# Kernel tuning notes

Measured on AMD Instinct MI355X. Metric: run time of the kernel, lower is better.

## Reference

```python
import jax, jax.numpy as jnp
import numpy as np

EPS = 1e-12  # keras K.l2_normalize epsilon


def _l2_normalize(v, axis):
    return v * jax.lax.rsqrt(jnp.maximum(jnp.sum(v * v, axis=axis, keepdims=True), EPS))


def setup_inputs() -> dict:
    key = jax.random.key(0)
    k1, k2, k3, k4 = jax.random.split(key, 4)
    B, T, D, K, O = 32, 1024, 512, 64, 1024
    x = jax.random.normal(k1, (B, T, D), dtype=jnp.float32)
    weight = jax.random.normal(k2, (D, K), dtype=jnp.float32) * (1.0 / np.sqrt(D))
    bias = jnp.zeros((K,), dtype=jnp.float32)
    centers = jax.random.normal(k3, (K, D), dtype=jnp.float32)
    reduc_dim = jax.random.normal(k4, (D * K, O), dtype=jnp.float32) * 0.01
    return {"x": x, "weight": weight, "bias": bias, "centers": centers, "reduc_dim": reduc_dim}


def reference(x, weight, bias, centers, reduc_dim):
    # x: [B,T,D], weight: [D,K], bias: [K]
    # soft assignment: softmax over centers
    a = jax.nn.softmax(jnp.einsum('btd,dk->btk', x, weight) + bias, axis=-1)  # [B,T,K]
    # aggregate descriptors per center: batch_dot over time axis -> [B,K,D]
    x_agg = jnp.einsum('btk,btd->bkd', a, x)
    # total soft weight per center: [B,K]
    sum_w = jnp.sum(a, axis=1)
    # residual vs centers, broadcast: [B,K,D]
    full = x_agg - sum_w[:, :, None] * centers[None, :, :]
    # intra-normalize per center vector
    full = _l2_normalize(full, axis=-1)
    B = x.shape[0]
    full = full.reshape(B, -1)  # [B, K*D]
    full = _l2_normalize(full, axis=-1)
    return full @ reduc_dim  # [B, output_dim]
```

## Files before the change

kernel.cpp:

```cpp
#include <hip/hip_runtime.h>
#include <math.h>

#define TT 1024
#define DD 512
#define KK 64
#define OO 1024
#define EPSF 1e-12f

typedef __attribute__((ext_vector_type(8))) short bf16x8;
typedef __attribute__((ext_vector_type(4))) float f32x4;

__device__ __forceinline__ ushort f2bf(float f) {
  unsigned u = __float_as_uint(f);
  u = (u + 0x7FFFu + ((u >> 16) & 1u)) >> 16;
  return (ushort)u;
}
__device__ __forceinline__ float bf2f(ushort h) {
  return __uint_as_float(((unsigned)h) << 16);
}


__global__ __launch_bounds__(256) void nv_k0(const float* __restrict__ w,
                                             ushort* __restrict__ whT,
                                             float* __restrict__ sum_w) {
  int idx = blockIdx.x * 256 + threadIdx.x;
  if (idx < 32768) {
    int d = idx >> 6, k = idx & 63;
    whT[(size_t)k * DD + d] = f2bf(w[idx]);
  } else if (idx < 32768 + 2048) {
    sum_w[idx - 32768] = 0.f;
  }
}

__global__ __launch_bounds__(256) void nv_k1(
    const float* __restrict__ x, const ushort* __restrict__ whT,
    const float* __restrict__ bias, ushort* __restrict__ aT,
    ushort* __restrict__ xbfT, float* __restrict__ sum_w) {
  const int b = blockIdx.y, t0 = blockIdx.x * 64;
  const int tid = threadIdx.x;
  const int wave = tid >> 6, lane = tid & 63, l15 = lane & 15, q = lane >> 4;

  __shared__ ushort xs[64 * 64];
  __shared__ ushort xsT[64 * 64];
  __shared__ ushort wsm[64 * 64];

  f32x4 acc[4];
#pragma unroll
  for (int nt = 0; nt < 4; ++nt)
#pragma unroll
    for (int r = 0; r < 4; ++r) acc[nt][r] = 0.f;

  for (int dc = 0; dc < DD; dc += 64) {
    __syncthreads();
#pragma unroll
    for (int it = 0; it < 2; ++it) {
      int gi = it * 256 + tid;
      int t = gi >> 3, gd = gi & 7;
      const float* px = x + (size_t)(b * TT + t0 + t) * DD + dc + gd * 8;
      float4 v0 = *(const float4*)px;
      float4 v1 = *(const float4*)(px + 4);
      ushort u[8];
      u[0] = f2bf(v0.x); u[1] = f2bf(v0.y); u[2] = f2bf(v0.z); u[3] = f2bf(v0.w);
      u[4] = f2bf(v1.x); u[5] = f2bf(v1.y); u[6] = f2bf(v1.z); u[7] = f2bf(v1.w);
      bf16x8 pk;
#pragma unroll
      for (int i = 0; i < 8; ++i) pk[i] = (short)u[i];
      *(bf16x8*)(xs + t * 64 + ((gd ^ (t & 7)) << 3)) = pk;
      int tg = t >> 3;
#pragma unroll
      for (int i = 0; i < 8; ++i) {
        int d = gd * 8 + i;
        xsT[d * 64 + ((tg ^ ((d >> 3) & 7)) << 3) + (t & 7)] = u[i];
      }
    }
#pragma unroll
    for (int it = 0; it < 2; ++it) {
      int gi = it * 256 + tid;
      int k = gi >> 3, gd = gi & 7;
      bf16x8 v = *(const bf16x8*)(whT + (size_t)k * DD + dc + gd * 8);
      *(bf16x8*)(wsm + k * 64 + ((gd ^ (k & 7)) << 3)) = v;
    }
    __syncthreads();
#pragma unroll
    for (int kc = 0; kc < 2; ++kc) {
      int gq = kc * 4 + q;
      int t = wave * 16 + l15;
      bf16x8 af = *(const bf16x8*)(xs + t * 64 + ((gq ^ (t & 7)) << 3));
#pragma unroll
      for (int nt = 0; nt < 4; ++nt) {
        int k = nt * 16 + l15;
        bf16x8 bfv = *(const bf16x8*)(wsm + k * 64 + ((gq ^ (k & 7)) << 3));
        acc[nt] = __builtin_amdgcn_mfma_f32_16x16x32_bf16(af, bfv, acc[nt], 0, 0, 0);
      }
    }
#pragma unroll
    for (int it = 0; it < 2; ++it) {
      int gi = it * 256 + tid;
      int d = gi >> 3, g = gi & 7;
      bf16x8 v = *(const bf16x8*)(xsT + d * 64 + (g << 3));
      int tg = g ^ ((d >> 3) & 7);
      *(bf16x8*)(xbfT + (size_t)(b * DD + dc + d) * TT + t0 + tg * 8) = v;
    }
  }

  float bia[4];
#pragma unroll
  for (int nt = 0; nt < 4; ++nt) bia[nt] = bias[nt * 16 + l15];

  ushort au[4][4];
  float sw[4] = {0.f, 0.f, 0.f, 0.f};
#pragma unroll
  for (int r = 0; r < 4; ++r) {
    float l[4];
#pragma unroll
    for (int nt = 0; nt < 4; ++nt) l[nt] = acc[nt][r] + bia[nt];
    float m = fmaxf(fmaxf(l[0], l[1]), fmaxf(l[2], l[3]));
#pragma unroll
    for (int s = 1; s <= 8; s <<= 1) m = fmaxf(m, __shfl_xor(m, s));
    float e[4];
#pragma unroll
    for (int nt = 0; nt < 4; ++nt) e[nt] = __expf(l[nt] - m);
    float ssum = e[0] + e[1] + e[2] + e[3];
#pragma unroll
    for (int s = 1; s <= 8; s <<= 1) ssum += __shfl_xor(ssum, s);
    float inv = 1.f / ssum;
#pragma unroll
    for (int nt = 0; nt < 4; ++nt) {
      ushort u = f2bf(e[nt] * inv);
      au[nt][r] = u;
      sw[nt] += bf2f(u);
    }
  }
#pragma unroll
  for (int nt = 0; nt < 4; ++nt) {
    float s = sw[nt];
    s += __shfl_xor(s, 16);
    s += __shfl_xor(s, 32);
    if (q == 0) atomicAdd(sum_w + b * KK + nt * 16 + l15, s);
  }
  __syncthreads();
#pragma unroll
  for (int nt = 0; nt < 4; ++nt)
#pragma unroll
    for (int r = 0; r < 4; ++r) {
      int k = nt * 16 + l15;
      int t = wave * 16 + q * 4 + r;
      xs[k * 64 + (((t >> 3) ^ (k & 7)) << 3) + (t & 7)] = au[nt][r];
    }
  __syncthreads();
#pragma unroll
  for (int it = 0; it < 2; ++it) {
    int gi = it * 256 + tid;
    int k = gi >> 3, g = gi & 7;
    bf16x8 v = *(const bf16x8*)(xs + k * 64 + (g << 3));
    int tg = g ^ (k & 7);
    *(bf16x8*)(aT + (size_t)(b * KK + k) * TT + t0 + tg * 8) = v;
  }
}

__global__ __launch_bounds__(256) void nv_k2(
    const ushort* __restrict__ aT, const ushort* __restrict__ xbfT,
    float* __restrict__ xaggP) {
  const int d0 = blockIdx.x * 64;
  const int b = blockIdx.y;
  const int tsp = blockIdx.z;
  const int tid = threadIdx.x;
  const int wave = tid >> 6, lane = tid & 63, l15 = lane & 15, q = lane >> 4;

  __shared__ ushort asx[64 * 64];
  __shared__ ushort xsb[64 * 64];

  f32x4 acc[4];
#pragma unroll
  for (int nt = 0; nt < 4; ++nt)
#pragma unroll
    for (int r = 0; r < 4; ++r) acc[nt][r] = 0.f;

  for (int tc = 0; tc < 4; ++tc) {
    const int t0 = tsp * 256 + tc * 64;
    __syncthreads();
#pragma unroll
    for (int it = 0; it < 2; ++it) {
      int gi = it * 256 + tid;
      int k = gi >> 3, g = gi & 7;
      bf16x8 v = *(const bf16x8*)(aT + (size_t)(b * KK + k) * TT + t0 + g * 8);
      *(bf16x8*)(asx + k * 64 + ((g ^ (k & 7)) << 3)) = v;
    }
#pragma unroll
    for (int it = 0; it < 2; ++it) {
      int gi = it * 256 + tid;
      int d = gi >> 3, g = gi & 7;
      bf16x8 v = *(const bf16x8*)(xbfT + (size_t)(b * DD + d0 + d) * TT + t0 + g * 8);
      *(bf16x8*)(xsb + d * 64 + ((g ^ (d & 7)) << 3)) = v;
    }
    __syncthreads();
#pragma unroll
    for (int kc = 0; kc < 2; ++kc) {
      int gq = kc * 4 + q;
      int k = wave * 16 + l15;
      bf16x8 af = *(const bf16x8*)(asx + k * 64 + ((gq ^ (k & 7)) << 3));
#pragma unroll
      for (int nt = 0; nt < 4; ++nt) {
        int d = nt * 16 + l15;
        bf16x8 bfv = *(const bf16x8*)(xsb + d * 64 + ((gq ^ (d & 7)) << 3));
        acc[nt] = __builtin_amdgcn_mfma_f32_16x16x32_bf16(af, bfv, acc[nt], 0, 0, 0);
      }
    }
  }
#pragma unroll
  for (int nt = 0; nt < 4; ++nt)
#pragma unroll
    for (int r = 0; r < 4; ++r) {
      int k = wave * 16 + q * 4 + r;
      xaggP[(size_t)((tsp * 32 + b) * KK + k) * DD + d0 + nt * 16 + l15] = acc[nt][r];
    }
}

__global__ __launch_bounds__(128) void nv_k3a(
    const float* __restrict__ xaggP, float* __restrict__ full,
    const float* __restrict__ centers, const float* __restrict__ sum_w,
    float* __restrict__ s1) {
  const int k = blockIdx.x, b = blockIdx.y;
  const int tid = threadIdx.x;
  const float sw = sum_w[b * KK + k];
  float4 v = make_float4(0.f, 0.f, 0.f, 0.f);
#pragma unroll
  for (int sp = 0; sp < 4; ++sp) {
    float4 p = *((const float4*)(xaggP + (size_t)((sp * 32 + b) * KK + k) * DD) + tid);
    v.x += p.x; v.y += p.y; v.z += p.z; v.w += p.w;
  }
  float4 c = *((const float4*)(centers + (size_t)k * DD) + tid);
  v.x = fmaf(-sw, c.x, v.x);
  v.y = fmaf(-sw, c.y, v.y);
  v.z = fmaf(-sw, c.z, v.z);
  v.w = fmaf(-sw, c.w, v.w);
  *((float4*)(full + (size_t)(b * KK + k) * DD) + tid) = v;
  float ss = v.x * v.x + v.y * v.y + v.z * v.z + v.w * v.w;
#pragma unroll
  for (int s = 1; s <= 32; s <<= 1) ss += __shfl_xor(ss, s);
  __shared__ float red[2];
  if ((tid & 63) == 0) red[tid >> 6] = ss;
  __syncthreads();
  if (tid == 0) s1[b * KK + k] = red[0] + red[1];
}

__global__ __launch_bounds__(64) void nv_k3b(const float* __restrict__ s1,
                                             float* __restrict__ scale) {
  const int b = blockIdx.x, k = threadIdx.x;
  float r = s1[b * KK + k];
  float d1 = fmaxf(r, EPSF);
  float s2 = r / d1;
#pragma unroll
  for (int s = 1; s <= 32; s <<= 1) s2 += __shfl_xor(s2, s);
  scale[b * KK + k] = rsqrtf(d1) * rsqrtf(fmaxf(s2, EPSF));
}

__global__ __launch_bounds__(128) void nv_k3c(const float* __restrict__ full,
                                              const float* __restrict__ scale,
                                              float* __restrict__ fullT) {
  const int blk = blockIdx.x;
  const int b = blk >> 6, k = blk & 63;
  const float sc = scale[blk];
  float4 v = *((const float4*)(full + (size_t)blk * DD) + threadIdx.x);
  int r0 = k * DD + threadIdx.x * 4;
  fullT[(size_t)(r0 + 0) * 32 + b] = v.x * sc;
  fullT[(size_t)(r0 + 1) * 32 + b] = v.y * sc;
  fullT[(size_t)(r0 + 2) * 32 + b] = v.z * sc;
  fullT[(size_t)(r0 + 3) * 32 + b] = v.w * sc;
}

__global__ __launch_bounds__(256, 2) void nv_k4(
    const float* __restrict__ fullT, const float* __restrict__ reduc,
    float* __restrict__ outP) {
  const int strip = blockIdx.x;
  const int ksp = blockIdx.y;
  const int tid = threadIdx.x;
  const int wave = tid >> 6, lane = tid & 63;
  const int c0 = strip * 256 + lane * 4;
  const int kblk = ksp * 256;

  __shared__ float fst[256 * 32];

#pragma unroll
  for (int it = 0; it < 8; ++it) {
    int f4 = it * 256 + tid;
    *(float4*)(fst + f4 * 4) = *(const float4*)(fullT + (size_t)kblk * 32 + f4 * 4);
  }
  __syncthreads();

  float4 acc[32];
#pragma unroll
  for (int b = 0; b < 32; ++b) acc[b] = make_float4(0.f, 0.f, 0.f, 0.f);

  const int kw = wave * 64;
#pragma unroll 2
  for (int kk = 0; kk < 64; ++kk) {
    const int kl = kw + kk;
    float4 rv = *(const float4*)(reduc + (size_t)(kblk + kl) * OO + c0);
#pragma unroll
    for (int b4 = 0; b4 < 8; ++b4) {
      float4 fv = *(const float4*)(fst + kl * 32 + b4 * 4);
      acc[b4 * 4 + 0].x = fmaf(fv.x, rv.x, acc[b4 * 4 + 0].x);
      acc[b4 * 4 + 0].y = fmaf(fv.x, rv.y, acc[b4 * 4 + 0].y);
      acc[b4 * 4 + 0].z = fmaf(fv.x, rv.z, acc[b4 * 4 + 0].z);
      acc[b4 * 4 + 0].w = fmaf(fv.x, rv.w, acc[b4 * 4 + 0].w);
      acc[b4 * 4 + 1].x = fmaf(fv.y, rv.x, acc[b4 * 4 + 1].x);
      acc[b4 * 4 + 1].y = fmaf(fv.y, rv.y, acc[b4 * 4 + 1].y);
      acc[b4 * 4 + 1].z = fmaf(fv.y, rv.z, acc[b4 * 4 + 1].z);
      acc[b4 * 4 + 1].w = fmaf(fv.y, rv.w, acc[b4 * 4 + 1].w);
      acc[b4 * 4 + 2].x = fmaf(fv.z, rv.x, acc[b4 * 4 + 2].x);
      acc[b4 * 4 + 2].y = fmaf(fv.z, rv.y, acc[b4 * 4 + 2].y);
      acc[b4 * 4 + 2].z = fmaf(fv.z, rv.z, acc[b4 * 4 + 2].z);
      acc[b4 * 4 + 2].w = fmaf(fv.z, rv.w, acc[b4 * 4 + 2].w);
      acc[b4 * 4 + 3].x = fmaf(fv.w, rv.x, acc[b4 * 4 + 3].x);
      acc[b4 * 4 + 3].y = fmaf(fv.w, rv.y, acc[b4 * 4 + 3].y);
      acc[b4 * 4 + 3].z = fmaf(fv.w, rv.z, acc[b4 * 4 + 3].z);
      acc[b4 * 4 + 3].w = fmaf(fv.w, rv.w, acc[b4 * 4 + 3].w);
    }
  }

  __syncthreads();
  for (int w = 0; w < 4; ++w) {
    if (wave == w) {
      if (w == 0) {
#pragma unroll
        for (int b = 0; b < 32; ++b)
          *(float4*)(fst + b * 256 + lane * 4) = acc[b];
      } else {
#pragma unroll
        for (int b = 0; b < 32; ++b) {
          float4 v = *(float4*)(fst + b * 256 + lane * 4);
          v.x += acc[b].x; v.y += acc[b].y; v.z += acc[b].z; v.w += acc[b].w;
          *(float4*)(fst + b * 256 + lane * 4) = v;
        }
      }
    }
    __syncthreads();
  }

#pragma unroll
  for (int it = 0; it < 8; ++it) {
    int f4 = it * 256 + tid;
    int b = f4 >> 6, cg = f4 & 63;
    *(float4*)(outP + ((size_t)(ksp * 32 + b) * OO) + strip * 256 + cg * 4) =
        *(const float4*)(fst + b * 256 + cg * 4);
  }
}

__global__ __launch_bounds__(256) void nv_k5(const float* __restrict__ outP,
                                             float* __restrict__ out) {
  const int idx = blockIdx.x * 256 + threadIdx.x;
  float s = 0.f;
#pragma unroll 8
  for (int sp = 0; sp < 128; ++sp) s += outP[(size_t)sp * 32768 + idx];
  out[idx] = s;
}

extern "C" void kernel_launch(void* const* d_in, const int* in_sizes, int n_in,
                              void* d_out, int out_size, void* d_ws, size_t ws_size,
                              hipStream_t stream) {
  const float* x = (const float*)d_in[0];
  const float* weight = (const float*)d_in[1];
  const float* bias = (const float*)d_in[2];
  const float* centers = (const float*)d_in[3];
  const float* reduc = (const float*)d_in[4];
  float* out = (float*)d_out;
  float* ws = (float*)d_ws;

  ushort* aT = (ushort*)ws;
  ushort* xbfT = (ushort*)(ws + 1048576);
  float* xaggP = ws + 9437184;
  float* full = ws + 13631488;
  float* fullT = ws + 14680064;
  float* outP = ws + 15728640;
  ushort* whT = (ushort*)(ws + 19922944);
  float* sum_w = ws + 19922944 + 16384;
  float* s1 = sum_w + 2048;
  float* scale = sum_w + 4096;

  nv_k0<<<136, 256, 0, stream>>>(weight, whT, sum_w);
  nv_k1<<<dim3(16, 32), 256, 0, stream>>>(x, whT, bias, aT, xbfT, sum_w);
  nv_k2<<<dim3(8, 32, 4), 256, 0, stream>>>(aT, xbfT, xaggP);
  nv_k3a<<<dim3(64, 32), 128, 0, stream>>>(xaggP, full, centers, sum_w, s1);
  nv_k3b<<<32, 64, 0, stream>>>(s1, scale);
  nv_k3c<<<2048, 128, 0, stream>>>(full, scale, fullT);
  nv_k4<<<dim3(4, 128), 256, 0, stream>>>(fullT, reduc, outP);
  nv_k5<<<128, 256, 0, stream>>>(outP, out);
}
```

Before: 293.3 us.

## Fuse soft-assignment and aggregation kernels, retile transpose, batch reduc loads

Merges the softmax-assignment kernel and the aggregation GEMM into one kernel. Each block keeps its assignment tile in shared memory and rereads x from global to build a transposed bf16 tile, so the aT and xbfT intermediates are no longer written and read through global memory. The time split doubles to 8 partials, and nv_k3a is widened to sum them. It also rewrites the transpose kernel to use a padded shared-memory tile for coalesced stores, loads four reduc rows per iteration in nv_k4 and drops its occupancy hint, and changes nv_k5 block size. The cost is fewer blocks for the fused kernel (256), reading x twice, and more xaggP partial traffic.

Result: no change. 290.3 us (-1.0%).

```diff
diff --git a/kernel.cpp b/kernel.cpp
--- a/kernel.cpp
+++ b/kernel.cpp
@@ -32,46 +32,43 @@
   }
 }
 
-__global__ __launch_bounds__(256) void nv_k1(
+__global__ __launch_bounds__(256) void nv_k12(
     const float* __restrict__ x, const ushort* __restrict__ whT,
-    const float* __restrict__ bias, ushort* __restrict__ aT,
-    ushort* __restrict__ xbfT, float* __restrict__ sum_w) {
-  const int b = blockIdx.y, t0 = blockIdx.x * 64;
+    const float* __restrict__ bias, float* __restrict__ xaggP,
+    float* __restrict__ sum_w) {
+  const int tsp = blockIdx.x, b = blockIdx.y;
+  const int t0 = tsp * 128;
   const int tid = threadIdx.x;
   const int wave = tid >> 6, lane = tid & 63, l15 = lane & 15, q = lane >> 4;
 
-  __shared__ ushort xs[64 * 64];
-  __shared__ ushort xsT[64 * 64];
+  __shared__ ushort xs[128 * 64];
   __shared__ ushort wsm[64 * 64];
-
-  f32x4 acc[4];
-#pragma unroll
-  for (int nt = 0; nt < 4; ++nt)
-#pragma unroll
-    for (int r = 0; r < 4; ++r) acc[nt][r] = 0.f;
+  __shared__ ushort aTl[64 * 128];
+  __shared__ ushort xsT[64 * 128];
+
+  f32x4 acc[2][4];
+#pragma unroll
+  for (int mt = 0; mt < 2; ++mt)
+#pragma unroll
+    for (int nt = 0; nt < 4; ++nt)
+#pragma unroll
+      for (int r = 0; r < 4; ++r) acc[mt][nt][r] = 0.f;
 
   for (int dc = 0; dc < DD; dc += 64) {
     __syncthreads();
 #pragma unroll
-    for (int it = 0; it < 2; ++it) {
+    for (int it = 0; it < 4; ++it) {
       int gi = it * 256 + tid;
       int t = gi >> 3, gd = gi & 7;
       const float* px = x + (size_t)(b * TT + t0 + t) * DD + dc + gd * 8;
       float4 v0 = *(const float4*)px;
       float4 v1 = *(const float4*)(px + 4);
-      ushort u[8];
-      u[0] = f2bf(v0.x); u[1] = f2bf(v0.y); u[2] = f2bf(v0.z); u[3] = f2bf(v0.w);
-      u[4] = f2bf(v1.x); u[5] = f2bf(v1.y); u[6] = f2bf(v1.z); u[7] = f2bf(v1.w);
       bf16x8 pk;
-#pragma unroll
-      for (int i = 0; i < 8; ++i) pk[i] = (short)u[i];
+      pk[0] = (short)f2bf(v0.x); pk[1] = (short)f2bf(v0.y);
+      pk[2] = (short)f2bf(v0.z); pk[3] = (short)f2bf(v0.w);
+      pk[4] = (short)f2bf(v1.x); pk[5] = (short)f2bf(v1.y);
+      pk[6] = (short)f2bf(v1.z); pk[7] = (short)f2bf(v1.w);
       *(bf16x8*)(xs + t * 64 + ((gd ^ (t & 7)) << 3)) = pk;
-      int tg = t >> 3;
-#pragma unroll
-      for (int i = 0; i < 8; ++i) {
-        int d = gd * 8 + i;
-        xsT[d * 64 + ((tg ^ ((d >> 3) & 7)) << 3) + (t & 7)] = u[i];
-      }
     }
 #pragma unroll
     for (int it = 0; it < 2; ++it) {
@@ -84,22 +81,20 @@
 #pragma unroll
     for (int kc = 0; kc < 2; ++kc) {
       int gq = kc * 4 + q;
-      int t = wave * 16 + l15;
-      bf16x8 af = *(const bf16x8*)(xs + t * 64 + ((gq ^ (t & 7)) << 3));
+      bf16x8 bfv[4];
 #pragma unroll
       for (int nt = 0; nt < 4; ++nt) {
         int k = nt * 16 + l15;
-        bf16x8 bfv = *(const bf16x8*)(wsm + k * 64 + ((gq ^ (k & 7)) << 3));
-        acc[nt] = __builtin_amdgcn_mfma_f32_16x16x32_bf16(af, bfv, acc[nt], 0, 0, 0);
-      }
-    }
-#pragma unroll
-    for (int it = 0; it < 2; ++it) {
-      int gi = it * 256 + tid;
-      int d = gi >> 3, g = gi & 7;
-      bf16x8 v = *(const bf16x8*)(xsT + d * 64 + (g << 3));
-      int tg = g ^ ((d >> 3) & 7);
-      *(bf16x8*)(xbfT + (size_t)(b * DD + dc + d) * TT + t0 + tg * 8) = v;
+        bfv[nt] = *(const bf16x8*)(wsm + k * 64 + ((gq ^ (k & 7)) << 3));
+      }
+#pragma unroll
+      for (int mt = 0; mt < 2; ++mt) {
+        int t = wave * 32 + mt * 16 + l15;
+        bf16x8 af = *(const bf16x8*)(xs + t * 64 + ((gq ^ (t & 7)) << 3));
+#pragma unroll
+        for (int nt = 0; nt < 4; ++nt)
+          acc[mt][nt] = __builtin_amdgcn_mfma_f32_16x16x32_bf16(af, bfv[nt], acc[mt][nt], 0, 0, 0);
+      }
     }
   }
 
@@ -107,30 +102,32 @@
 #pragma unroll
   for (int nt = 0; nt < 4; ++nt) bia[nt] = bias[nt * 16 + l15];
 
-  ushort au[4][4];
+  ushort au[2][4][4];
   float sw[4] = {0.f, 0.f, 0.f, 0.f};
 #pragma unroll
-  for (int r = 0; r < 4; ++r) {
-    float l[4];
-#pragma unroll
-    for (int nt = 0; nt < 4; ++nt) l[nt] = acc[nt][r] + bia[nt];
-    float m = fmaxf(fmaxf(l[0], l[1]), fmaxf(l[2], l[3]));
-#pragma unroll
-    for (int s = 1; s <= 8; s <<= 1) m = fmaxf(m, __shfl_xor(m, s));
-    float e[4];
-#pragma unroll
-    for (int nt = 0; nt < 4; ++nt) e[nt] = __expf(l[nt] - m);
-    float ssum = e[0] + e[1] + e[2] + e[3];
-#pragma unroll
-    for (int s = 1; s <= 8; s <<= 1) ssum += __shfl_xor(ssum, s);
-    float inv = 1.f / ssum;
-#pragma unroll
-    for (int nt = 0; nt < 4; ++nt) {
-      ushort u = f2bf(e[nt] * inv);
-      au[nt][r] = u;
-      sw[nt] += bf2f(u);
-    }
-  }
+  for (int mt = 0; mt < 2; ++mt)
+#pragma unroll
+    for (int r = 0; r < 4; ++r) {
+      float l[4];
+#pragma unroll
+      for (int nt = 0; nt < 4; ++nt) l[nt] = acc[mt][nt][r] + bia[nt];
+      float m = fmaxf(fmaxf(l[0], l[1]), fmaxf(l[2], l[3]));
+#pragma unroll
+      for (int s = 1; s <= 8; s <<= 1) m = fmaxf(m, __shfl_xor(m, s));
+      float e[4];
+#pragma unroll
+      for (int nt = 0; nt < 4; ++nt) e[nt] = __expf(l[nt] - m);
+      float ssum = e[0] + e[1] + e[2] + e[3];
+#pragma unroll
+      for (int s = 1; s <= 8; s <<= 1) ssum += __shfl_xor(ssum, s);
+      float inv = 1.f / ssum;
+#pragma unroll
+      for (int nt = 0; nt < 4; ++nt) {
+        ushort u = f2bf(e[nt] * inv);
+        au[mt][nt][r] = u;
+        sw[nt] += bf2f(u);
+      }
+    }
 #pragma unroll
   for (int nt = 0; nt < 4; ++nt) {
     float s = sw[nt];
@@ -138,82 +135,66 @@
     s += __shfl_xor(s, 32);
     if (q == 0) atomicAdd(sum_w + b * KK + nt * 16 + l15, s);
   }
-  __syncthreads();
-#pragma unroll
-  for (int nt = 0; nt < 4; ++nt)
-#pragma unroll
-    for (int r = 0; r < 4; ++r) {
-      int k = nt * 16 + l15;
-      int t = wave * 16 + q * 4 + r;
-      xs[k * 64 + (((t >> 3) ^ (k & 7)) << 3) + (t & 7)] = au[nt][r];
-    }
-  __syncthreads();
-#pragma unroll
-  for (int it = 0; it < 2; ++it) {
-    int gi = it * 256 + tid;
-    int k = gi >> 3, g = gi & 7;
-    bf16x8 v = *(const bf16x8*)(xs + k * 64 + (g << 3));
-    int tg = g ^ (k & 7);
-    *(bf16x8*)(aT + (size_t)(b * KK + k) * TT + t0 + tg * 8) = v;
-  }
-}
-
-__global__ __launch_bounds__(256) void nv_k2(
-    const ushort* __restrict__ aT, const ushort* __restrict__ xbfT,
-    float* __restrict__ xaggP) {
-  const int d0 = blockIdx.x * 64;
-  const int b = blockIdx.y;
-  const int tsp = blockIdx.z;
-  const int tid = threadIdx.x;
-  const int wave = tid >> 6, lane = tid & 63, l15 = lane & 15, q = lane >> 4;
-
-  __shared__ ushort asx[64 * 64];
-  __shared__ ushort xsb[64 * 64];
-
-  f32x4 acc[4];
-#pragma unroll
-  for (int nt = 0; nt < 4; ++nt)
-#pragma unroll
-    for (int r = 0; r < 4; ++r) acc[nt][r] = 0.f;
-
-  for (int tc = 0; tc < 4; ++tc) {
-    const int t0 = tsp * 256 + tc * 64;
-    __syncthreads();
-#pragma unroll
-    for (int it = 0; it < 2; ++it) {
-      int gi = it * 256 + tid;
-      int k = gi >> 3, g = gi & 7;
-      bf16x8 v = *(const bf16x8*)(aT + (size_t)(b * KK + k) * TT + t0 + g * 8);
-      *(bf16x8*)(asx + k * 64 + ((g ^ (k & 7)) << 3)) = v;
-    }
-#pragma unroll
-    for (int it = 0; it < 2; ++it) {
-      int gi = it * 256 + tid;
-      int d = gi >> 3, g = gi & 7;
-      bf16x8 v = *(const bf16x8*)(xbfT + (size_t)(b * DD + d0 + d) * TT + t0 + g * 8);
-      *(bf16x8*)(xsb + d * 64 + ((g ^ (d & 7)) << 3)) = v;
-    }
-    __syncthreads();
-#pragma unroll
-    for (int kc = 0; kc < 2; ++kc) {
-      int gq = kc * 4 + q;
-      int k = wave * 16 + l15;
-      bf16x8 af = *(const bf16x8*)(asx + k * 64 + ((gq ^ (k & 7)) << 3));
-#pragma unroll
-      for (int nt = 0; nt < 4; ++nt) {
-        int d = nt * 16 + l15;
-        bf16x8 bfv = *(const bf16x8*)(xsb + d * 64 + ((gq ^ (d & 7)) << 3));
-        acc[nt] = __builtin_amdgcn_mfma_f32_16x16x32_bf16(af, bfv, acc[nt], 0, 0, 0);
-      }
-    }
-  }
-#pragma unroll
-  for (int nt = 0; nt < 4; ++nt)
-#pragma unroll
-    for (int r = 0; r < 4; ++r) {
-      int k = wave * 16 + q * 4 + r;
-      xaggP[(size_t)((tsp * 32 + b) * KK + k) * DD + d0 + nt * 16 + l15] = acc[nt][r];
-    }
+#pragma unroll
+  for (int mt = 0; mt < 2; ++mt)
+#pragma unroll
+    for (int nt = 0; nt < 4; ++nt)
+#pragma unroll
+      for (int r = 0; r < 4; ++r) {
+        int k = nt * 16 + l15;
+        int t = wave * 32 + mt * 16 + q * 4 + r;
+        aTl[k * 128 + (((t >> 3) ^ (k & 15)) << 3) + (t & 7)] = au[mt][nt][r];
+      }
+  __syncthreads();
+
+  bf16x8 afB[4][4];
+#pragma unroll
+  for (int mk = 0; mk < 4; ++mk)
+#pragma unroll
+    for (int ks = 0; ks < 4; ++ks) {
+      int k = mk * 16 + l15;
+      int g = ks * 4 + q;
+      afB[mk][ks] = *(const bf16x8*)(aTl + k * 128 + ((g ^ (k & 15)) << 3));
+    }
+
+  for (int dc = 0; dc < DD; dc += 64) {
+    __syncthreads();
+#pragma unroll
+    for (int it = 0; it < 8; ++it) {
+      int fi = it * 256 + tid;
+      int t = fi >> 4, dq = fi & 15;
+      float4 v = *(const float4*)(x + (size_t)(b * TT + t0 + t) * DD + dc + dq * 4);
+      int tg = t >> 3;
+      float vv[4] = {v.x, v.y, v.z, v.w};
+#pragma unroll
+      for (int i = 0; i < 4; ++i) {
+        int d = dq * 4 + i;
+        xsT[d * 128 + ((tg ^ (d & 15)) << 3) + (t & 7)] = f2bf(vv[i]);
+      }
+    }
+    __syncthreads();
+    f32x4 accB[4];
+#pragma unroll
+    for (int mk = 0; mk < 4; ++mk)
+#pragma unroll
+      for (int r = 0; r < 4; ++r) accB[mk][r] = 0.f;
+#pragma unroll
+    for (int ks = 0; ks < 4; ++ks) {
+      int d = wave * 16 + l15;
+      int g = ks * 4 + q;
+      bf16x8 bfv = *(const bf16x8*)(xsT + d * 128 + ((g ^ (d & 15)) << 3));
+#pragma unroll
+      for (int mk = 0; mk < 4; ++mk)
+        accB[mk] = __builtin_amdgcn_mfma_f32_16x16x32_bf16(afB[mk][ks], bfv, accB[mk], 0, 0, 0);
+    }
+#pragma unroll
+    for (int mk = 0; mk < 4; ++mk)
+#pragma unroll
+      for (int r = 0; r < 4; ++r) {
+        int k = mk * 16 + q * 4 + r;
+        xaggP[(size_t)((tsp * 32 + b) * KK + k) * DD + dc + wave * 16 + l15] = accB[mk][r];
+      }
+  }
 }
 
 __global__ __launch_bounds__(128) void nv_k3a(
@@ -225,7 +206,7 @@
   const float sw = sum_w[b * KK + k];
   float4 v = make_float4(0.f, 0.f, 0.f, 0.f);
 #pragma unroll
-  for (int sp = 0; sp < 4; ++sp) {
+  for (int sp = 0; sp < 8; ++sp) {
     float4 p = *((const float4*)(xaggP + (size_t)((sp * 32 + b) * KK + k) * DD) + tid);
     v.x += p.x; v.y += p.y; v.z += p.z; v.w += p.w;
   }
@@ -255,21 +236,37 @@
   scale[b * KK + k] = rsqrtf(d1) * rsqrtf(fmaxf(s2, EPSF));
 }
 
-__global__ __launch_bounds__(128) void nv_k3c(const float* __restrict__ full,
+__global__ __launch_bounds__(256) void nv_k3c(const float* __restrict__ full,
                                               const float* __restrict__ scale,
                                               float* __restrict__ fullT) {
-  const int blk = blockIdx.x;
-  const int b = blk >> 6, k = blk & 63;
-  const float sc = scale[blk];
-  float4 v = *((const float4*)(full + (size_t)blk * DD) + threadIdx.x);
-  int r0 = k * DD + threadIdx.x * 4;
-  fullT[(size_t)(r0 + 0) * 32 + b] = v.x * sc;
-  fullT[(size_t)(r0 + 1) * 32 + b] = v.y * sc;
-  fullT[(size_t)(r0 + 2) * 32 + b] = v.z * sc;
-  fullT[(size_t)(r0 + 3) * 32 + b] = v.w * sc;
-}
-
-__global__ __launch_bounds__(256, 2) void nv_k4(
+  const int k = blockIdx.x, d0 = blockIdx.y * 128;
+  const int tid = threadIdx.x;
+  __shared__ float ls[32 * 132];
+
+#pragma unroll
+  for (int it = 0; it < 4; ++it) {
+    int fi = it * 256 + tid;
+    int b = fi >> 5, dg = fi & 31;
+    float sc = scale[b * KK + k];
+    float4 v = *((const float4*)(full + (size_t)(b * KK + k) * DD + d0) + dg);
+    v.x *= sc; v.y *= sc; v.z *= sc; v.w *= sc;
+    *(float4*)(ls + b * 132 + dg * 4) = v;
+  }
+  __syncthreads();
+#pragma unroll
+  for (int it = 0; it < 4; ++it) {
+    int fo = it * 256 + tid;
+    int d = fo >> 3, bq = fo & 7;
+    float4 v;
+    v.x = ls[(bq * 4 + 0) * 132 + d];
+    v.y = ls[(bq * 4 + 1) * 132 + d];
+    v.z = ls[(bq * 4 + 2) * 132 + d];
+    v.w = ls[(bq * 4 + 3) * 132 + d];
+    *(float4*)(fullT + (size_t)(k * DD + d0 + d) * 32 + bq * 4) = v;
+  }
+}
+
+__global__ __launch_bounds__(256) void nv_k4(
     const float* __restrict__ fullT, const float* __restrict__ reduc,
     float* __restrict__ outP) {
   const int strip = blockIdx.x;
@@ -293,29 +290,34 @@
   for (int b = 0; b < 32; ++b) acc[b] = make_float4(0.f, 0.f, 0.f, 0.f);
 
   const int kw = wave * 64;
-#pragma unroll 2
-  for (int kk = 0; kk < 64; ++kk) {
-    const int kl = kw + kk;
-    float4 rv = *(const float4*)(reduc + (size_t)(kblk + kl) * OO + c0);
-#pragma unroll
-    for (int b4 = 0; b4 < 8; ++b4) {
-      float4 fv = *(const float4*)(fst + kl * 32 + b4 * 4);
-      acc[b4 * 4 + 0].x = fmaf(fv.x, rv.x, acc[b4 * 4 + 0].x);
-      acc[b4 * 4 + 0].y = fmaf(fv.x, rv.y, acc[b4 * 4 + 0].y);
-      acc[b4 * 4 + 0].z = fmaf(fv.x, rv.z, acc[b4 * 4 + 0].z);
-      acc[b4 * 4 + 0].w = fmaf(fv.x, rv.w, acc[b4 * 4 + 0].w);
-      acc[b4 * 4 + 1].x = fmaf(fv.y, rv.x, acc[b4 * 4 + 1].x);
-      acc[b4 * 4 + 1].y = fmaf(fv.y, rv.y, acc[b4 * 4 + 1].y);
-      acc[b4 * 4 + 1].z = fmaf(fv.y, rv.z, acc[b4 * 4 + 1].z);
-      acc[b4 * 4 + 1].w = fmaf(fv.y, rv.w, acc[b4 * 4 + 1].w);
-      acc[b4 * 4 + 2].x = fmaf(fv.z, rv.x, acc[b4 * 4 + 2].x);
-      acc[b4 * 4 + 2].y = fmaf(fv.z, rv.y, acc[b4 * 4 + 2].y);
-      acc[b4 * 4 + 2].z = fmaf(fv.z, rv.z, acc[b4 * 4 + 2].z);
-      acc[b4 * 4 + 2].w = fmaf(fv.z, rv.w, acc[b4 * 4 + 2].w);
-      acc[b4 * 4 + 3].x = fmaf(fv.w, rv.x, acc[b4 * 4 + 3].x);
-      acc[b4 * 4 + 3].y = fmaf(fv.w, rv.y, acc[b4 * 4 + 3].y);
-      acc[b4 * 4 + 3].z = fmaf(fv.w, rv.z, acc[b4 * 4 + 3].z);
-      acc[b4 * 4 + 3].w = fmaf(fv.w, rv.w, acc[b4 * 4 + 3].w);
+  for (int kk = 0; kk < 64; kk += 4) {
+    float4 rv[4];
+#pragma unroll
+    for (int j = 0; j < 4; ++j)
+      rv[j] = *(const float4*)(reduc + (size_t)(kblk + kw + kk + j) * OO + c0);
+#pragma unroll
+    for (int j = 0; j < 4; ++j) {
+      const int kl = kw + kk + j;
+#pragma unroll
+      for (int b4 = 0; b4 < 8; ++b4) {
+        float4 fv = *(const float4*)(fst + kl * 32 + b4 * 4);
+        acc[b4 * 4 + 0].x = fmaf(fv.x, rv[j].x, acc[b4 * 4 + 0].x);
+        acc[b4 * 4 + 0].y = fmaf(fv.x, rv[j].y, acc[b4 * 4 + 0].y);
+        acc[b4 * 4 + 0].z = fmaf(fv.x, rv[j].z, acc[b4 * 4 + 0].z);
+        acc[b4 * 4 + 0].w = fmaf(fv.x, rv[j].w, acc[b4 * 4 + 0].w);
+        acc[b4 * 4 + 1].x = fmaf(fv.y, rv[j].x, acc[b4 * 4 + 1].x);
+        acc[b4 * 4 + 1].y = fmaf(fv.y, rv[j].y, acc[b4 * 4 + 1].y);
+        acc[b4 * 4 + 1].z = fmaf(fv.y, rv[j].z, acc[b4 * 4 + 1].z);
+        acc[b4 * 4 + 1].w = fmaf(fv.y, rv[j].w, acc[b4 * 4 + 1].w);
+        acc[b4 * 4 + 2].x = fmaf(fv.z, rv[j].x, acc[b4 * 4 + 2].x);
+        acc[b4 * 4 + 2].y = fmaf(fv.z, rv[j].y, acc[b4 * 4 + 2].y);
+        acc[b4 * 4 + 2].z = fmaf(fv.z, rv[j].z, acc[b4 * 4 + 2].z);
+        acc[b4 * 4 + 2].w = fmaf(fv.z, rv[j].w, acc[b4 * 4 + 2].w);
+        acc[b4 * 4 + 3].x = fmaf(fv.w, rv[j].x, acc[b4 * 4 + 3].x);
+        acc[b4 * 4 + 3].y = fmaf(fv.w, rv[j].y, acc[b4 * 4 + 3].y);
+        acc[b4 * 4 + 3].z = fmaf(fv.w, rv[j].z, acc[b4 * 4 + 3].z);
+        acc[b4 * 4 + 3].w = fmaf(fv.w, rv[j].w, acc[b4 * 4 + 3].w);
+      }
     }
   }
 
@@ -347,9 +349,9 @@
   }
 }
 
-__global__ __launch_bounds__(256) void nv_k5(const float* __restrict__ outP,
+__global__ __launch_bounds__(128) void nv_k5(const float* __restrict__ outP,
                                              float* __restrict__ out) {
-  const int idx = blockIdx.x * 256 + threadIdx.x;
+  const int idx = blockIdx.x * 128 + threadIdx.x;
   float s = 0.f;
 #pragma unroll 8
   for (int sp = 0; sp < 128; ++sp) s += outP[(size_t)sp * 32768 + idx];
@@ -367,23 +369,20 @@
   float* out = (float*)d_out;
   float* ws = (float*)d_ws;
 
-  ushort* aT = (ushort*)ws;
-  ushort* xbfT = (ushort*)(ws + 1048576);
-  float* xaggP = ws + 9437184;
-  float* full = ws + 13631488;
-  float* fullT = ws + 14680064;
-  float* outP = ws + 15728640;
-  ushort* whT = (ushort*)(ws + 19922944);
-  float* sum_w = ws + 19922944 + 16384;
+  float* xaggP = ws;
+  float* full = ws + 8388608;
+  float* fullT = ws + 9437184;
+  float* outP = ws + 10485760;
+  ushort* whT = (ushort*)(ws + 14680064);
+  float* sum_w = ws + 14696448;
   float* s1 = sum_w + 2048;
   float* scale = sum_w + 4096;
 
   nv_k0<<<136, 256, 0, stream>>>(weight, whT, sum_w);
-  nv_k1<<<dim3(16, 32), 256, 0, stream>>>(x, whT, bias, aT, xbfT, sum_w);
-  nv_k2<<<dim3(8, 32, 4), 256, 0, stream>>>(aT, xbfT, xaggP);
+  nv_k12<<<dim3(8, 32), 256, 0, stream>>>(x, whT, bias, xaggP, sum_w);
   nv_k3a<<<dim3(64, 32), 128, 0, stream>>>(xaggP, full, centers, sum_w, s1);
   nv_k3b<<<32, 64, 0, stream>>>(s1, scale);
-  nv_k3c<<<2048, 128, 0, stream>>>(full, scale, fullT);
+  nv_k3c<<<dim3(64, 4), 256, 0, stream>>>(full, scale, fullT);
   nv_k4<<<dim3(4, 128), 256, 0, stream>>>(fullT, reduc, outP);
-  nv_k5<<<128, 256, 0, stream>>>(outP, out);
-}
+  nv_k5<<<256, 128, 0, stream>>>(outP, out);
+}
```
